# Kernel optimization log

Measured on AMD Instinct MI355X. Metric: run time of the kernel, lower is better.

## Reference

```python
import jax, jax.numpy as jnp
import numpy as np
from jax import lax

N = 4096  # minibatch size / number of points


def _pairwise_dist(x):
    # x: (N, d) -> (N, N) euclidean distance matrix, symmetric, zero diagonal
    sq = jnp.sum(x * x, axis=-1)
    d2 = sq[:, None] + sq[None, :] - 2.0 * (x @ x.T)
    d2 = jnp.maximum(d2, 0.0)
    d = jnp.sqrt(d2)
    return d * (1.0 - jnp.eye(x.shape[0], dtype=x.dtype))


def setup_inputs() -> dict:
    key = jax.random.key(0)
    k1, k2 = jax.random.split(key)
    x_in = jax.random.normal(k1, (N, 32), dtype=jnp.float32)   # input-space points
    x_lat = jax.random.normal(k2, (N, 8), dtype=jnp.float32)   # latent-space points
    return {
        "input_distances": _pairwise_dist(x_in),
        "latent_distances": _pairwise_dist(x_lat),
    }


def _mst_edges(D):
    """Prim's algorithm on a dense distance matrix.

    Returns (N-1, 2) int32 edges (parent_in_tree, new_node). With distinct
    edge weights (random point clouds) the MST is unique, so this matches
    the original union-find/Kruskal get_mst_edges(one_root=True) edge set.
    """
    n = D.shape[0]
    in_tree0 = jnp.zeros((n,), dtype=bool).at[0].set(True)
    dist0 = D[0]                          # best distance from tree to each node
    parent0 = jnp.zeros((n,), dtype=jnp.int32)

    def step(carry, _):
        dist, parent, in_tree = carry
        masked = jnp.where(in_tree, jnp.inf, dist)
        j = jnp.argmin(masked).astype(jnp.int32)  # nearest non-tree node
        edge = jnp.stack([parent[j], j])
        in_tree = in_tree.at[j].set(True)
        row = D[j]                         # relax: distances via new node j
        better = row < dist
        dist = jnp.where(better, row, dist)
        parent = jnp.where(better, j, parent)
        return (dist, parent, in_tree), edge

    _, edges = lax.scan(step, (dist0, parent0, in_tree0), None, length=n - 1)
    return edges  # (N-1, 2)


def _select(D, pairs):
    return D[pairs[:, 0], pairs[:, 1]]


def reference(input_distances, latent_distances):
    pairs1 = _mst_edges(input_distances)
    pairs2 = _mst_edges(latent_distances)
    sig1 = _select(input_distances, pairs1)
    sig2 = _select(latent_distances, pairs2)
    sig1_2 = _select(latent_distances, pairs1)
    sig2_1 = _select(input_distances, pairs2)
    distance1_2 = jnp.sum((sig1 - sig1_2) ** 2)
    distance2_1 = jnp.sum((sig2 - sig2_1) ** 2)
    return distance1_2 + distance2_1
```

## Files before the change

kernel.cpp:

```cpp
#include <hip/hip_runtime.h>
#include <stdint.h>


#define NPTS 4096
#define NCHUNK 64
#define NBLK 1024
#define ROUNDS 12

typedef unsigned long long u64;
typedef float nfloat4 __attribute__((ext_vector_type(4)));

__device__ __forceinline__ u64 umin64(u64 a, u64 b) { return a < b ? a : b; }

__device__ __forceinline__ u64 pack_edge(float w, int i, int j) {
    unsigned wb = __float_as_uint(w);
    int u = i < j ? i : j;
    int v = i < j ? j : i;
    return ((u64)wb << 24) | ((u64)(unsigned)u << 12) | (u64)(unsigned)v;
}

__device__ __forceinline__ u64 wave_min64(u64 v) {
    #pragma unroll
    for (int off = 32; off; off >>= 1)
        v = umin64(v, __shfl_down(v, (unsigned)off, 64));
    return v;
}

__global__ __launch_bounds__(256) void cold_k(
    const float* __restrict__ D1, const float* __restrict__ D2,
    u64* __restrict__ best, u64* __restrict__ cand,
    int* __restrict__ done, float* __restrict__ out) {
    if (blockIdx.x == 0 && threadIdx.x == 0) {
        done[0] = 0; done[1] = 0; out[0] = 0.f;
    }
    int pb = blockIdx.x >> 10;
    int rb = blockIdx.x & (NBLK - 1);
    const float* __restrict__ D = pb ? D2 : D1;
    u64* __restrict__ bst = best + pb * NPTS;
    u64* __restrict__ cnd = cand + (size_t)pb * NPTS * NCHUNK;

    int wave = threadIdx.x >> 6, lane = threadIdx.x & 63;
    int i = rb * 4 + wave;
    const nfloat4* __restrict__ row = (const nfloat4*)(D + (size_t)i * NPTS);

    u64 m = ~0ull;
    #pragma unroll
    for (int k = 0; k < 16; ++k) {
        nfloat4 w = row[k * 64 + lane];
        int j0 = k * 256 + lane * 4;
        #pragma unroll
        for (int q = 0; q < 4; ++q)
            if (j0 + q != i) m = umin64(m, pack_edge(w[q], i, j0 + q));
    }
    cnd[i * NCHUNK + lane] = m;
    u64 bv = wave_min64(m);
    if (lane == 0) bst[i] = bv;
}

__global__ __launch_bounds__(256) void warm_k(
    const float* __restrict__ D1, const float* __restrict__ D2,
    u64* __restrict__ best, const int* __restrict__ comp,
    const int* __restrict__ done, u64* __restrict__ cand) {
    int pb = blockIdx.x >> 10;
    if (done[pb]) return;
    int rb = blockIdx.x & (NBLK - 1);
    const float* __restrict__ D = pb ? D2 : D1;
    const int* __restrict__ cmpg = comp + pb * NPTS;
    u64* __restrict__ bst = best + pb * NPTS;
    u64* __restrict__ cnd = cand + (size_t)pb * NPTS * NCHUNK;

    int wave = threadIdx.x >> 6, lane = threadIdx.x & 63;
    int i = rb * 4 + wave;
    int ci = cmpg[i];

    u64 live = ~0ull;
    u64 c = cnd[i * NCHUNK + lane];
    if (c != ~0ull) {
        int u = (int)((c >> 12) & 0xFFF), v = (int)(c & 0xFFF);
        int j = (u == i) ? v : u;
        if (cmpg[j] != ci) {
            live = c;
        } else {
            const nfloat4* __restrict__ row =
                (const nfloat4*)(D + (size_t)i * NPTS);
            u64 m = ~0ull;
            #pragma unroll 4
            for (int k = 0; k < 16; ++k) {
                nfloat4 w = row[k * 64 + lane];
                int j0 = k * 256 + lane * 4;
                int4 cj = *(const int4*)&cmpg[j0];
                if (cj.x != ci) m = umin64(m, pack_edge(w.x, i, j0));
                if (cj.y != ci) m = umin64(m, pack_edge(w.y, i, j0 + 1));
                if (cj.z != ci) m = umin64(m, pack_edge(w.z, i, j0 + 2));
                if (cj.w != ci) m = umin64(m, pack_edge(w.w, i, j0 + 3));
            }
            cnd[i * NCHUNK + lane] = m;
            live = m;
        }
    }
    u64 rmin = wave_min64(live);
    if (lane == 0 && rmin != ~0ull && rmin < bst[ci]) atomicMin(&bst[ci], rmin);
}

__global__ __launch_bounds__(1024) void contract_k(
    const float* __restrict__ D1, const float* __restrict__ D2,
    u64* __restrict__ best, int* __restrict__ comp,
    int* __restrict__ done, float* __restrict__ out, int identity) {
    int pb = blockIdx.x;
    if (!identity && done[pb]) return;
    u64* __restrict__ bst = best + pb * NPTS;
    int* __restrict__ cmp = comp + pb * NPTS;

    __shared__ int link_s[NPTS];
    __shared__ float red_s[16];
    __shared__ int flag_s;
    int t = threadIdx.x;
    float loss = 0.f;

    int eu[4], ev[4], nl[4];
    bool act[4];

    for (int q = 0; q < 4; ++q) {
        int c = t + q * 1024;
        u64 b = bst[c];
        bool a = (b != ~0ull);
        act[q] = a;
        int u = (int)((b >> 12) & 0xFFF), v = (int)(b & 0xFFF);
        eu[q] = u; ev[q] = v;
        int l = c;
        if (a) {
            if (identity) l = (u == c) ? v : u;
            else { int cu = cmp[u]; l = (cu == c) ? cmp[v] : cu; }
        }
        link_s[c] = l;
    }
    __syncthreads();

    for (int q = 0; q < 4; ++q) {
        int c = t + q * 1024;
        int l = link_s[c];
        bool is2 = (l != c) && (link_s[l] == c);
        if (act[q] && !(is2 && c > l)) {
            size_t off = (size_t)eu[q] * NPTS + ev[q];
            float d = D1[off] - D2[off];
            loss += d * d;
        }
        nl[q] = (is2 && c < l) ? c : l;
    }
    __syncthreads();
    for (int q = 0; q < 4; ++q) link_s[t + q * 1024] = nl[q];
    __syncthreads();

    for (int it = 0; it < 13; ++it) {
        if (t == 0) flag_s = 0;
        __syncthreads();
        bool ch = false;
        for (int q = 0; q < 4; ++q) {
            int c = t + q * 1024;
            int l = link_s[c];
            int ll = link_s[l];
            nl[q] = ll;
            ch |= (ll != l);
        }
        if (ch) flag_s = 1;
        __syncthreads();
        for (int q = 0; q < 4; ++q) link_s[t + q * 1024] = nl[q];
        __syncthreads();
        if (!flag_s) break;
    }

    int c0 = identity ? 0 : cmp[0];
    __syncthreads();
    int root0 = link_s[c0];
    int same = 1;
    for (int q = 0; q < 4; ++q) {
        int v = t + q * 1024;
        int oc = identity ? v : cmp[v];
        int r = link_s[oc];
        cmp[v] = r;
        same &= (r == root0);
        bst[v] = ~0ull;
    }
    int all = __syncthreads_and(same);
    if (all && t == 0) done[pb] = 1;

    #pragma unroll
    for (int off = 32; off; off >>= 1) loss += __shfl_down(loss, (unsigned)off, 64);
    int wave = t >> 6, lane = t & 63;
    if (lane == 0) red_s[wave] = loss;
    __syncthreads();
    if (t == 0) {
        float s = 0.f;
        for (int wv = 0; wv < 16; ++wv) s += red_s[wv];
        atomicAdd(out, s);
    }
}

extern "C" void kernel_launch(void* const* d_in, const int* in_sizes, int n_in,
                              void* d_out, int out_size, void* d_ws, size_t ws_size,
                              hipStream_t stream) {
    const float* D1 = (const float*)d_in[0];
    const float* D2 = (const float*)d_in[1];
    float* out = (float*)d_out;

    char* ws = (char*)d_ws;
    u64* best = (u64*)ws;
    int* comp = (int*)(ws + 65536);
    int* done = (int*)(ws + 65536 + 32768);
    u64* cand = (u64*)(ws + 98312);

    cold_k<<<2 * NBLK, 256, 0, stream>>>(D1, D2, best, cand, done, out);
    contract_k<<<2, 1024, 0, stream>>>(D1, D2, best, comp, done, out, 1);
    for (int r = 1; r < ROUNDS; ++r) {
        warm_k<<<2 * NBLK, 256, 0, stream>>>(D1, D2, best, comp, done, cand);
        contract_k<<<2, 1024, 0, stream>>>(D1, D2, best, comp, done, out, 0);
    }
}
```

Before: 166.5 us.

## Use symmetric tiled chunk minima and rescan only stale chunks in warm rounds

```diff
diff --git a/kernel.cpp b/kernel.cpp
--- a/kernel.cpp
+++ b/kernel.cpp
@@ -8,7 +8,6 @@
 #define ROUNDS 12
 
 typedef unsigned long long u64;
-typedef float nfloat4 __attribute__((ext_vector_type(4)));
 
 __device__ __forceinline__ u64 umin64(u64 a, u64 b) { return a < b ? a : b; }
 
@@ -26,35 +25,72 @@
     return v;
 }
 
-__global__ __launch_bounds__(256) void cold_k(
+__global__ __launch_bounds__(256) void tile_k(
     const float* __restrict__ D1, const float* __restrict__ D2,
-    u64* __restrict__ best, u64* __restrict__ cand,
+    u64* __restrict__ cand) {
+    int pb = blockIdx.x >> 12;
+    int t  = blockIdx.x & 4095;
+    int r = t >> 6, c = t & 63;
+    if (r > c) return;
+    const float* __restrict__ D = pb ? D2 : D1;
+    u64* __restrict__ cnd = cand + (size_t)pb * NPTS * NCHUNK;
+
+    __shared__ float ts[64][65];
+    int R0 = r << 6, C0 = c << 6;
+    int tid = threadIdx.x;
+
+    #pragma unroll
+    for (int e = 0; e < 4; ++e) {
+        int idx4 = tid + e * 256;
+        int row = idx4 >> 4, c4 = idx4 & 15;
+        const float4* __restrict__ rp =
+            (const float4*)(D + (size_t)(R0 + row) * NPTS + C0);
+        float4 w = rp[c4];
+        ts[row][c4 * 4    ] = w.x; ts[row][c4 * 4 + 1] = w.y;
+        ts[row][c4 * 4 + 2] = w.z; ts[row][c4 * 4 + 3] = w.w;
+    }
+    __syncthreads();
+
+    int wave = tid >> 6, lane = tid & 63;
+    if (wave == 0) {
+        int i = R0 + lane;
+        float wm = 3.4e38f; int jm = 0;
+        if (r == c) {
+            for (int j = 0; j < 64; ++j) {
+                float x = ts[lane][j];
+                if ((C0 + j) != i && x < wm) { wm = x; jm = C0 + j; }
+            }
+        } else {
+            for (int j = 0; j < 64; ++j) {
+                float x = ts[lane][j];
+                if (x < wm) { wm = x; jm = C0 + j; }
+            }
+        }
+        cnd[i * NCHUNK + c] = pack_edge(wm, i, jm);
+    } else if (wave == 1 && r != c) {
+        int jcol = C0 + lane;
+        float wm = 3.4e38f; int im = 0;
+        for (int k2 = 0; k2 < 64; ++k2) {
+            float x = ts[k2][lane];
+            if (x < wm) { wm = x; im = R0 + k2; }
+        }
+        cnd[jcol * NCHUNK + r] = pack_edge(wm, jcol, im);
+    }
+}
+
+__global__ __launch_bounds__(256) void finalize_k(
+    u64* __restrict__ best, const u64* __restrict__ cand,
     int* __restrict__ done, float* __restrict__ out) {
     if (blockIdx.x == 0 && threadIdx.x == 0) {
         done[0] = 0; done[1] = 0; out[0] = 0.f;
     }
     int pb = blockIdx.x >> 10;
     int rb = blockIdx.x & (NBLK - 1);
-    const float* __restrict__ D = pb ? D2 : D1;
-    u64* __restrict__ bst = best + pb * NPTS;
-    u64* __restrict__ cnd = cand + (size_t)pb * NPTS * NCHUNK;
-
+    const u64* __restrict__ cnd = cand + (size_t)pb * NPTS * NCHUNK;
     int wave = threadIdx.x >> 6, lane = threadIdx.x & 63;
     int i = rb * 4 + wave;
-    const nfloat4* __restrict__ row = (const nfloat4*)(D + (size_t)i * NPTS);
-
-    u64 m = ~0ull;
-    #pragma unroll
-    for (int k = 0; k < 16; ++k) {
-        nfloat4 w = row[k * 64 + lane];
-        int j0 = k * 256 + lane * 4;
-        #pragma unroll
-        for (int q = 0; q < 4; ++q)
-            if (j0 + q != i) m = umin64(m, pack_edge(w[q], i, j0 + q));
-    }
-    cnd[i * NCHUNK + lane] = m;
-    u64 bv = wave_min64(m);
-    if (lane == 0) bst[i] = bv;
+    u64 bv = wave_min64(cnd[i * NCHUNK + lane]);
+    if (lane == 0) best[pb * NPTS + i] = bv;
 }
 
 __global__ __launch_bounds__(256) void warm_k(
@@ -74,31 +110,49 @@
     int ci = cmpg[i];
 
     u64 live = ~0ull;
+    bool dead = false;
     u64 c = cnd[i * NCHUNK + lane];
     if (c != ~0ull) {
         int u = (int)((c >> 12) & 0xFFF), v = (int)(c & 0xFFF);
         int j = (u == i) ? v : u;
-        if (cmpg[j] != ci) {
-            live = c;
-        } else {
-            const nfloat4* __restrict__ row =
-                (const nfloat4*)(D + (size_t)i * NPTS);
-            u64 m = ~0ull;
-            #pragma unroll 4
-            for (int k = 0; k < 16; ++k) {
-                nfloat4 w = row[k * 64 + lane];
-                int j0 = k * 256 + lane * 4;
-                int4 cj = *(const int4*)&cmpg[j0];
-                if (cj.x != ci) m = umin64(m, pack_edge(w.x, i, j0));
-                if (cj.y != ci) m = umin64(m, pack_edge(w.y, i, j0 + 1));
-                if (cj.z != ci) m = umin64(m, pack_edge(w.z, i, j0 + 2));
-                if (cj.w != ci) m = umin64(m, pack_edge(w.w, i, j0 + 3));
-            }
-            cnd[i * NCHUNK + lane] = m;
-            live = m;
-        }
-    }
-    u64 rmin = wave_min64(live);
+        if (cmpg[j] != ci) live = c;
+        else dead = true;
+    }
+
+    u64 extra = ~0ull;
+    u64 mask = __ballot(dead);
+    if (mask) {
+        const float4* __restrict__ rowf = (const float4*)(D + (size_t)i * NPTS);
+        const int4* __restrict__ cmp4 = (const int4*)cmpg;
+        int g = lane >> 4, m16 = lane & 15;
+        while (mask) {
+            int kq = -1;
+            #pragma unroll
+            for (int s = 0; s < 4; ++s) {
+                int kk = mask ? (int)(__ffsll((long long)mask) - 1) : -1;
+                if (kk >= 0) mask &= mask - 1;
+                if (s == g) kq = kk;
+            }
+            u64 e = ~0ull;
+            if (kq >= 0) {
+                float4 w = rowf[kq * 16 + m16];
+                int4 cj = cmp4[kq * 16 + m16];
+                int j0 = kq * 64 + m16 * 4;
+                if (cj.x != ci) e = umin64(e, pack_edge(w.x, i, j0));
+                if (cj.y != ci) e = umin64(e, pack_edge(w.y, i, j0 + 1));
+                if (cj.z != ci) e = umin64(e, pack_edge(w.z, i, j0 + 2));
+                if (cj.w != ci) e = umin64(e, pack_edge(w.w, i, j0 + 3));
+            }
+            #pragma unroll
+            for (int off = 8; off; off >>= 1)
+                e = umin64(e, __shfl_down(e, (unsigned)off, 16));
+            if (kq >= 0 && m16 == 0) {
+                cnd[i * NCHUNK + kq] = e;
+                extra = umin64(extra, e);
+            }
+        }
+    }
+    u64 rmin = wave_min64(umin64(live, extra));
     if (lane == 0 && rmin != ~0ull && rmin < bst[ci]) atomicMin(&bst[ci], rmin);
 }
 
@@ -209,7 +263,8 @@
     int* done = (int*)(ws + 65536 + 32768);
     u64* cand = (u64*)(ws + 98312);
 
-    cold_k<<<2 * NBLK, 256, 0, stream>>>(D1, D2, best, cand, done, out);
+    tile_k<<<2 * 4096, 256, 0, stream>>>(D1, D2, cand);
+    finalize_k<<<2 * NBLK, 256, 0, stream>>>(best, cand, done, out);
     contract_k<<<2, 1024, 0, stream>>>(D1, D2, best, comp, done, out, 1);
     for (int r = 1; r < ROUNDS; ++r) {
         warm_k<<<2 * NBLK, 256, 0, stream>>>(D1, D2, best, comp, done, cand);
```

Result: faster. 136.5 us (-18.0%).
